# Kernel tuning notes

Measured on AMD Instinct MI355X. Metric: run time of the kernel, lower is better.

## Reference

```python
import jax, jax.numpy as jnp
import numpy as np

B, S, I, H = 32, 512, 512, 1024

def _xavier(key, shape):
    fan_in, fan_out = shape[0], shape[1]
    a = jnp.sqrt(6.0 / (fan_in + fan_out))
    return jax.random.uniform(key, shape, jnp.float32, -a, a)

def setup_inputs() -> dict:
    key = jax.random.key(0)
    ks = jax.random.split(key, 10)
    inp = {
        'x': jax.random.normal(ks[0], (B, S, I), jnp.float32),
        'h0': jnp.zeros((B, H), jnp.float32),
        'c0': jnp.zeros((B, H), jnp.float32),
        'W_ii': _xavier(ks[1], (I, H)), 'W_hi': _xavier(ks[2], (H, H)), 'b_i': jnp.zeros((H,), jnp.float32),
        'W_if': _xavier(ks[3], (I, H)), 'W_hf': _xavier(ks[4], (H, H)), 'b_f': jnp.zeros((H,), jnp.float32),
        'W_ig': _xavier(ks[5], (I, H)), 'W_hg': _xavier(ks[6], (H, H)), 'b_g': jnp.zeros((H,), jnp.float32),
        'W_io': _xavier(ks[7], (I, H)), 'W_ho': _xavier(ks[8], (H, H)), 'b_o': jnp.zeros((H,), jnp.float32),
    }
    return inp

def _lstm(x, h0, c0, W_ii, W_hi, b_i, W_if, W_hf, b_f, W_ig, W_hg, b_g, W_io, W_ho, b_o):
    # Precompute input-to-hidden projections for all timesteps (big fused GEMMs).
    xi = jnp.einsum('bsi,ih->sbh', x, W_ii) + b_i  # (S,B,H)
    xf = jnp.einsum('bsi,ih->sbh', x, W_if) + b_f
    xg = jnp.einsum('bsi,ih->sbh', x, W_ig) + b_g
    xo = jnp.einsum('bsi,ih->sbh', x, W_io) + b_o

    def step(carry, gates_t):
        h, c = carry
        xi_t, xf_t, xg_t, xo_t = gates_t
        i_t = jax.nn.sigmoid(xi_t + h @ W_hi)
        f_t = jax.nn.sigmoid(xf_t + h @ W_hf)
        g_t = jnp.tanh(xg_t + h @ W_hg)
        o_t = jax.nn.sigmoid(xo_t + h @ W_ho)
        c_new = f_t * c + i_t * g_t
        h_new = o_t * jnp.tanh(c_new)
        return (h_new, c_new), (h_new, f_t, i_t, o_t, g_t, c_new)

    (hT, cT), (hs, fs, is_, os, gs, cs) = jax.lax.scan(step, (h0, c0), (xi, xf, xg, xo))
    hidden_seq = jnp.transpose(hs, (1, 0, 2))  # (B,S,H)
    return hidden_seq, hT, cT, fs, is_, os, gs, cs

def reference(x, h0, c0, W_ii, W_hi, b_i, W_if, W_hf, b_f, W_ig, W_hg, b_g, W_io, W_ho, b_o):
    return _lstm(x, h0, c0, W_ii, W_hi, b_i, W_if, W_hf, b_f, W_ig, W_hg, b_g, W_io, W_ho, b_o)
```

## Files before the change

kernel.cpp:

```cpp
#include <hip/hip_runtime.h>
#include <stdint.h>

#define S_LEN 512
#define BATCH 32
#define IDIM 512
#define HDIM 1024
#define NBLK 64

typedef __attribute__((ext_vector_type(8))) short bf16x8;
typedef __attribute__((ext_vector_type(4))) float f32x4;

typedef const __attribute__((address_space(1))) unsigned int as1_uint;
typedef __attribute__((address_space(3))) unsigned int as3_uint;

__device__ __forceinline__ unsigned short f2bf(float f) {
  unsigned int u = __float_as_uint(f);
  u = (u + 0x7fffu + ((u >> 16) & 1u)) >> 16;
  return (unsigned short)u;
}

__device__ __forceinline__ void gld_lds16(const void* g, void* l) {
  __builtin_amdgcn_global_load_lds((as1_uint*)g, (as3_uint*)l, 16, 0, 0);
}

__device__ __forceinline__ float sigm(float x) { return 1.f / (1.f + __expf(-x)); }
__device__ __forceinline__ float tanh_f(float x) { return 1.f - 2.f / (__expf(2.f * x) + 1.f); }

__global__ void k_cast_x(const float* __restrict__ src, unsigned short* __restrict__ dst, int n8) {
  int i0 = blockIdx.x * blockDim.x + threadIdx.x;
  int stride = gridDim.x * blockDim.x;
  for (int i = i0; i < n8; i += stride) {
    const float4* s4 = (const float4*)(src + (size_t)i * 8);
    float4 a = s4[0], b = s4[1];
    bf16x8 v;
    v[0] = (short)f2bf(a.x); v[1] = (short)f2bf(a.y); v[2] = (short)f2bf(a.z); v[3] = (short)f2bf(a.w);
    v[4] = (short)f2bf(b.x); v[5] = (short)f2bf(b.y); v[6] = (short)f2bf(b.z); v[7] = (short)f2bf(b.w);
    *(bf16x8*)(dst + (size_t)i * 8) = v;
  }
}

__global__ void k_tcast_w(const float* __restrict__ src, unsigned short* __restrict__ dst, int K) {
  __shared__ float t[64][65];
  int k0 = blockIdx.x * 64, h0 = blockIdx.y * 64;
  int tid = threadIdx.x;
#pragma unroll 4
  for (int j = 0; j < 16; ++j) {
    int idx = j * 256 + tid;
    int kl = idx >> 6, hl = idx & 63;
    t[kl][hl] = src[(size_t)(k0 + kl) * HDIM + h0 + hl];
  }
  __syncthreads();
  int hl = tid >> 2, kg = tid & 3;
  unsigned short* drow = dst + (size_t)(h0 + hl) * K + k0 + kg * 16;
#pragma unroll
  for (int jj = 0; jj < 4; ++jj) {
    ushort4 v;
    v.x = f2bf(t[kg * 16 + jj * 4 + 0][hl]);
    v.y = f2bf(t[kg * 16 + jj * 4 + 1][hl]);
    v.z = f2bf(t[kg * 16 + jj * 4 + 2][hl]);
    v.w = f2bf(t[kg * 16 + jj * 4 + 3][hl]);
    *(ushort4*)(drow + jj * 4) = v;
  }
}

__global__ __launch_bounds__(256) void k_proj(
    const unsigned short* __restrict__ xb, const unsigned short* __restrict__ wib,
    const float* __restrict__ b_i, const float* __restrict__ b_f,
    const float* __restrict__ b_g, const float* __restrict__ b_o,
    float* __restrict__ Xi, float* __restrict__ Xf, float* __restrict__ Xg,
    float* __restrict__ Xo) {
  __shared__ unsigned short As[128 * 64];
  __shared__ unsigned short Bs[128 * 64];
  int tid = threadIdx.x;
  int l = tid & 63, w = tid >> 6;
  int mt = blockIdx.x >> 5, nt = blockIdx.x & 31;
  int m0 = mt * 128, n0 = nt * 128;
  int g = nt >> 3;
  int wm = (w >> 1) * 64, wn = (w & 1) * 64;

  f32x4 acc[4][4];
  for (int mi = 0; mi < 4; ++mi)
    for (int ni = 0; ni < 4; ++ni)
      for (int r = 0; r < 4; ++r) acc[mi][ni][r] = 0.f;

  for (int kt = 0; kt < 8; ++kt) {
    int k0 = kt * 64;
#pragma unroll
    for (int j = 0; j < 4; ++j) {
      int idx = j * 256 + tid;
      int row = idx >> 3, c = idx & 7;
      int sc = c ^ (row & 7);
      gld_lds16(xb + (size_t)(m0 + row) * IDIM + k0 + sc * 8,
                (char*)As + ((j * 256 + (w << 6)) << 4));
      gld_lds16(wib + (size_t)(n0 + row) * IDIM + k0 + sc * 8,
                (char*)Bs + ((j * 256 + (w << 6)) << 4));
    }
    __syncthreads();
#pragma unroll
    for (int kst = 0; kst < 2; ++kst) {
      bf16x8 af[4], bfr[4];
#pragma unroll
      for (int mi = 0; mi < 4; ++mi) {
        int row = wm + mi * 16 + (l & 15);
        int c = (kst << 2) + (l >> 4);
        af[mi] = *(const bf16x8*)((const char*)As + row * 128 + ((c ^ (row & 7)) << 4));
      }
#pragma unroll
      for (int ni = 0; ni < 4; ++ni) {
        int row = wn + ni * 16 + (l & 15);
        int c = (kst << 2) + (l >> 4);
        bfr[ni] = *(const bf16x8*)((const char*)Bs + row * 128 + ((c ^ (row & 7)) << 4));
      }
#pragma unroll
      for (int mi = 0; mi < 4; ++mi)
#pragma unroll
        for (int ni = 0; ni < 4; ++ni)
          acc[mi][ni] = __builtin_amdgcn_mfma_f32_16x16x32_bf16(af[mi], bfr[ni], acc[mi][ni], 0, 0, 0);
    }
    __syncthreads();
  }

  const float* bias = g == 0 ? b_i : g == 1 ? b_f : g == 2 ? b_g : b_o;
  float* dst = g == 0 ? Xi : g == 1 ? Xf : g == 2 ? Xg : Xo;
#pragma unroll
  for (int ni = 0; ni < 4; ++ni) {
    int n = n0 + wn + ni * 16 + (l & 15);
    int h = n & 1023;
    float bv = bias[h];
#pragma unroll
    for (int mi = 0; mi < 4; ++mi)
#pragma unroll
      for (int r = 0; r < 4; ++r) {
        int m = m0 + wm + mi * 16 + ((l >> 4) << 2) + r;
        int b = m >> 9, s = m & 511;
        dst[(size_t)(s * BATCH + b) * HDIM + h] = acc[mi][ni][r] + bv;
      }
  }
}

__global__ __launch_bounds__(256, 1) void k_rnn(
    const unsigned short* __restrict__ whb, const float* __restrict__ h0,
    const float* __restrict__ c0, char* __restrict__ hbufA,
    char* __restrict__ hbufB, unsigned int* __restrict__ cnt,
    const float* __restrict__ Xi, const float* __restrict__ Xf,
    const float* __restrict__ Xg, const float* __restrict__ Xo,
    float* __restrict__ csw, float* __restrict__ hseq, float* __restrict__ hT,
    float* __restrict__ cT) {
  __shared__ char lds[40960];
  const int ACT = 32768;

  const int tid = threadIdx.x;
  const int w = tid >> 6, l = tid & 63;
  const int ln = l & 15, lk = l >> 4;
  const int bid = blockIdx.x;

  float* isw = (float*)Xi; float* fsw = (float*)Xf;
  float* gsw = (float*)Xg; float* osw = (float*)Xo;
  const float* XW = (w == 0) ? Xi : (w == 1) ? Xf : (w == 2) ? Xg : Xo;

  bf16x8 Breg[4][8];
#pragma unroll
  for (int g = 0; g < 4; ++g)
#pragma unroll
    for (int j = 0; j < 8; ++j)
      Breg[g][j] = *(const bf16x8*)(whb + (((size_t)(g << 10) + (bid << 4) + ln) << 10) +
                                    ((w << 3) + j) * 32 + (lk << 3));

  const int b = tid >> 3, hp = tid & 7;
  const int gh = (bid << 4) + (hp << 1);
  const int fks = gh >> 5, fmt = b >> 4;
  const int flk = ((gh & 31) >> 3);
  const int foff = (((fks << 1) + fmt) << 10) + (flk << 8) + ((b & 15) << 4) + ((hp & 3) << 2);

  float2 c = *(const float2*)&c0[((size_t)b << 10) + gh];

  {
    float2 hv = *(const float2*)&h0[((size_t)b << 10) + gh];
    unsigned int pv = (unsigned int)f2bf(hv.x) | ((unsigned int)f2bf(hv.y) << 16);
    __hip_atomic_store((unsigned int*)(hbufA + foff), pv, __ATOMIC_RELAXED,
                       __HIP_MEMORY_SCOPE_AGENT);
    asm volatile("s_waitcnt vmcnt(0)" ::: "memory");
    __syncthreads();
    if (tid == 0)
      __hip_atomic_fetch_add(cnt + ((bid & 7) << 5), 1u, __ATOMIC_RELAXED,
                             __HIP_MEMORY_SCOPE_AGENT);
  }

  for (int t = 0; t < S_LEN; ++t) {
    const char* hin = (t & 1) ? hbufB : hbufA;
    char* hout = (t & 1) ? hbufA : hbufB;

    float xp[2][4];
    {
      const float* xb_ = XW + (((size_t)(t << 5)) << 10) + (bid << 4) + ln;
#pragma unroll
      for (int mt = 0; mt < 2; ++mt)
#pragma unroll
        for (int r = 0; r < 4; ++r)
          xp[mt][r] = xb_[((size_t)((mt << 4) + (lk << 2) + r)) << 10];
    }

    {
      const unsigned int need = 8u * (unsigned int)(t + 1);
      const unsigned int* cp = cnt + ((l & 7) << 5);
      while (true) {
        unsigned int v = __hip_atomic_load(cp, __ATOMIC_RELAXED, __HIP_MEMORY_SCOPE_AGENT);
        if (__all((l < 8) ? (int)(v >= need) : 1)) break;
        __builtin_amdgcn_s_sleep(1);
      }
    }
    __builtin_amdgcn_sched_barrier(0);

    bf16x8 a[8][2];
#pragma unroll
    for (int j = 0; j < 8; ++j)
#pragma unroll
      for (int mt = 0; mt < 2; ++mt) {
        const char* ap = hin + (((((w << 3) + j) << 1) + mt) << 10) + (l << 4);
        asm volatile("global_load_dwordx4 %0, %1, off sc0 sc1"
                     : "=v"(a[j][mt]) : "v"(ap) : "memory");
      }
    asm volatile("s_waitcnt vmcnt(0)" ::: "memory");
    __builtin_amdgcn_sched_barrier(0);

    f32x4 acc[4][2];
#pragma unroll
    for (int g = 0; g < 4; ++g)
#pragma unroll
      for (int mt = 0; mt < 2; ++mt)
#pragma unroll
        for (int r = 0; r < 4; ++r) acc[g][mt][r] = 0.f;
#pragma unroll
    for (int j = 0; j < 8; ++j)
#pragma unroll
      for (int mt = 0; mt < 2; ++mt)
#pragma unroll
        for (int g = 0; g < 4; ++g)
          acc[g][mt] = __builtin_amdgcn_mfma_f32_16x16x32_bf16(a[j][mt], Breg[g][j],
                                                               acc[g][mt], 0, 0, 0);

#pragma unroll
    for (int g = 0; g < 4; ++g)
#pragma unroll
      for (int mt = 0; mt < 2; ++mt)
        *(f32x4*)(lds + (((((w << 2) + g) << 1) + mt) << 10) + (l << 4)) = acc[g][mt];
    __syncthreads();

#pragma unroll
    for (int mt = 0; mt < 2; ++mt) {
      f32x4 s = *(const f32x4*)(lds + ((((0 * 4 + w) << 1) + mt) << 10) + (l << 4));
#pragma unroll
      for (int kw = 1; kw < 4; ++kw) {
        f32x4 p = *(const f32x4*)(lds + ((((kw * 4 + w) << 1) + mt) << 10) + (l << 4));
#pragma unroll
        for (int r = 0; r < 4; ++r) s[r] += p[r];
      }
#pragma unroll
      for (int r = 0; r < 4; ++r) {
        float pre = s[r] + xp[mt][r];
        float act = (w == 2) ? tanh_f(pre) : sigm(pre);
        *(float*)(lds + ACT + ((((w << 5) + (mt << 4) + (lk << 2) + r) << 4) + ln) * 4) = act;
      }
    }
    __syncthreads();

    float2 iv = *(const float2*)(lds + ACT + ((((0 << 5) + b) << 4) + (hp << 1)) * 4);
    float2 fv = *(const float2*)(lds + ACT + ((((1 << 5) + b) << 4) + (hp << 1)) * 4);
    float2 gv = *(const float2*)(lds + ACT + ((((2 << 5) + b) << 4) + (hp << 1)) * 4);
    float2 ov = *(const float2*)(lds + ACT + ((((3 << 5) + b) << 4) + (hp << 1)) * 4);

    c.x = fv.x * c.x + iv.x * gv.x;
    c.y = fv.y * c.y + iv.y * gv.y;
    float h0v = ov.x * tanh_f(c.x), h1v = ov.y * tanh_f(c.y);

    if (t < S_LEN - 1) {
      unsigned int pv = (unsigned int)f2bf(h0v) | ((unsigned int)f2bf(h1v) << 16);
      __hip_atomic_store((unsigned int*)(hout + foff), pv, __ATOMIC_RELAXED,
                         __HIP_MEMORY_SCOPE_AGENT);
      asm volatile("s_waitcnt vmcnt(0)" ::: "memory");
      __syncthreads();
      if (tid == 0)
        __hip_atomic_fetch_add(cnt + ((bid & 7) << 5), 1u, __ATOMIC_RELAXED,
                               __HIP_MEMORY_SCOPE_AGENT);
    }

    size_t oo = (((size_t)(t << 5) + b) << 10) + gh;
    *(float2*)(isw + oo) = iv;
    *(float2*)(fsw + oo) = fv;
    *(float2*)(gsw + oo) = gv;
    *(float2*)(osw + oo) = ov;
    *(float2*)(csw + oo) = c;
    *(float2*)(hseq + (((size_t)(b << 9) + t) << 10) + gh) = make_float2(h0v, h1v);
    if (t == S_LEN - 1) {
      *(float2*)(hT + (((size_t)b) << 10) + gh) = make_float2(h0v, h1v);
      *(float2*)(cT + (((size_t)b) << 10) + gh) = c;
    }
  }
}

extern "C" void kernel_launch(void* const* d_in, const int* in_sizes, int n_in,
                              void* d_out, int out_size, void* d_ws, size_t ws_size,
                              hipStream_t stream) {
  const float* x = (const float*)d_in[0];
  const float* h0 = (const float*)d_in[1];
  const float* c0 = (const float*)d_in[2];
  const float* Wi[4] = {(const float*)d_in[3], (const float*)d_in[6], (const float*)d_in[9], (const float*)d_in[12]};
  const float* Wh[4] = {(const float*)d_in[4], (const float*)d_in[7], (const float*)d_in[10], (const float*)d_in[13]};
  const float* bias[4] = {(const float*)d_in[5], (const float*)d_in[8], (const float*)d_in[11], (const float*)d_in[14]};

  float* out = (float*)d_out;
  float* R0 = out;
  float* R1 = out + 16777216;
  float* R2 = R1 + 32768;
  float* R3 = R2 + 32768;
  float* R4 = R3 + 16777216;
  float* R5 = R4 + 16777216;
  float* R6 = R5 + 16777216;
  float* R7 = R6 + 16777216;
  float* Xg_[4] = {R4, R3, R6, R5};

  char* ws = (char*)d_ws;
  unsigned short* whb = (unsigned short*)ws;
  unsigned short* wib = (unsigned short*)(ws + 8388608);
  char* hbufA = ws + 12582912;
  char* hbufB = ws + 12648448;
  unsigned int* cnt = (unsigned int*)(ws + 12713984);

  unsigned short* xb = (unsigned short*)R0;

  hipMemsetAsync(cnt, 0, 1024, stream);
  k_cast_x<<<2048, 256, 0, stream>>>(x, xb, (BATCH * S_LEN * IDIM) / 8);
  for (int g = 0; g < 4; ++g) {
    k_tcast_w<<<dim3(8, 16), 256, 0, stream>>>(Wi[g], wib + (size_t)g * 1024 * 512, 512);
    k_tcast_w<<<dim3(16, 16), 256, 0, stream>>>(Wh[g], whb + (size_t)g * 1024 * 1024, 1024);
  }
  k_proj<<<4096, 256, 0, stream>>>(xb, wib, bias[0], bias[1], bias[2], bias[3],
                                   Xg_[0], Xg_[1], Xg_[2], Xg_[3]);
  k_rnn<<<NBLK, 256, 0, stream>>>(whb, h0, c0, hbufA, hbufB, cnt,
                                  Xg_[0], Xg_[1], Xg_[2], Xg_[3],
                                  R7, R0, R1, R2);
}
```

Measured before the change: 2.119 ms.

## Split recurrent LSTM work by batch halves so blocks sync in smaller groups

Each block now handles 16 batch rows and 32 hidden units across all four gates, instead of all 32 batch rows and 16 hidden units. Block parity selects the batch half. Each block waits only on the four counters for its own batch half rather than all eight, and reads half as much h from the exchange buffer per step. The cost is twice as many resident weight registers, which are pinned to AGPRs through an asm constraint. The activation staging area is also padded to a row stride of 34 floats to cut LDS bank conflicts.

New measurement: 1.945 ms. 8.2% less time.

```diff
diff --git a/kernel.cpp b/kernel.cpp
--- a/kernel.cpp
+++ b/kernel.cpp
@@ -146,44 +146,54 @@
     const float* __restrict__ Xg, const float* __restrict__ Xo,
     float* __restrict__ csw, float* __restrict__ hseq, float* __restrict__ hT,
     float* __restrict__ cT) {
-  __shared__ char lds[40960];
+  __shared__ char lds[41472];
   const int ACT = 32768;
 
   const int tid = threadIdx.x;
   const int w = tid >> 6, l = tid & 63;
   const int ln = l & 15, lk = l >> 4;
   const int bid = blockIdx.x;
+  const int dm = bid & 1, hb = bid >> 1;
 
   float* isw = (float*)Xi; float* fsw = (float*)Xf;
   float* gsw = (float*)Xg; float* osw = (float*)Xo;
   const float* XW = (w == 0) ? Xi : (w == 1) ? Xf : (w == 2) ? Xg : Xo;
 
-  bf16x8 Breg[4][8];
+  bf16x8 Breg[8][8];
 #pragma unroll
   for (int g = 0; g < 4; ++g)
 #pragma unroll
+    for (int hh = 0; hh < 2; ++hh)
+#pragma unroll
+      for (int j = 0; j < 8; ++j) {
+        const size_t row = (size_t)((g << 10) + (hb << 5) + (hh << 4) + ln);
+        Breg[g * 2 + hh][j] =
+            *(const bf16x8*)(whb + (row << 10) + (w << 8) + (j << 5) + (lk << 3));
+      }
+#pragma unroll
+  for (int nt = 0; nt < 8; ++nt)
+#pragma unroll
     for (int j = 0; j < 8; ++j)
-      Breg[g][j] = *(const bf16x8*)(whb + (((size_t)(g << 10) + (bid << 4) + ln) << 10) +
-                                    ((w << 3) + j) * 32 + (lk << 3));
-
-  const int b = tid >> 3, hp = tid & 7;
-  const int gh = (bid << 4) + (hp << 1);
-  const int fks = gh >> 5, fmt = b >> 4;
-  const int flk = ((gh & 31) >> 3);
-  const int foff = (((fks << 1) + fmt) << 10) + (flk << 8) + ((b & 15) << 4) + ((hp & 3) << 2);
-
-  float2 c = *(const float2*)&c0[((size_t)b << 10) + gh];
+      asm volatile("" : "+a"(Breg[nt][j]));
+
+  const int pb = tid >> 4, hp = tid & 15;
+  const int bg = (dm << 4) + pb;
+  const int gh = (hb << 5) + (hp << 1);
+  const int o = hp << 1;
+  const int foff = (dm << 15) + (hb << 10) + ((o >> 3) << 8) + (pb << 4) + ((o & 7) << 1);
+  unsigned int* const myflag = cnt + (((dm << 2) + (hb & 3)) << 5);
+
+  float2 c = *(const float2*)&c0[((size_t)bg << 10) + gh];
 
   {
-    float2 hv = *(const float2*)&h0[((size_t)b << 10) + gh];
+    float2 hv = *(const float2*)&h0[((size_t)bg << 10) + gh];
     unsigned int pv = (unsigned int)f2bf(hv.x) | ((unsigned int)f2bf(hv.y) << 16);
     __hip_atomic_store((unsigned int*)(hbufA + foff), pv, __ATOMIC_RELAXED,
                        __HIP_MEMORY_SCOPE_AGENT);
     asm volatile("s_waitcnt vmcnt(0)" ::: "memory");
     __syncthreads();
     if (tid == 0)
-      __hip_atomic_fetch_add(cnt + ((bid & 7) << 5), 1u, __ATOMIC_RELAXED,
-                             __HIP_MEMORY_SCOPE_AGENT);
+      __hip_atomic_fetch_add(myflag, 1u, __ATOMIC_RELAXED, __HIP_MEMORY_SCOPE_AGENT);
   }
 
   for (int t = 0; t < S_LEN; ++t) {
@@ -192,82 +202,76 @@
 
     float xp[2][4];
     {
-      const float* xb_ = XW + (((size_t)(t << 5)) << 10) + (bid << 4) + ln;
-#pragma unroll
-      for (int mt = 0; mt < 2; ++mt)
+      const float* xb_ = XW + ((size_t)((t << 5) + (dm << 4)) << 10) + (hb << 5) + ln;
+#pragma unroll
+      for (int hh = 0; hh < 2; ++hh)
 #pragma unroll
         for (int r = 0; r < 4; ++r)
-          xp[mt][r] = xb_[((size_t)((mt << 4) + (lk << 2) + r)) << 10];
+          xp[hh][r] = xb_[((size_t)((lk << 2) + r) << 10) + (hh << 4)];
     }
 
     {
       const unsigned int need = 8u * (unsigned int)(t + 1);
-      const unsigned int* cp = cnt + ((l & 7) << 5);
+      const unsigned int* cp = cnt + (((dm << 2) + (l & 3)) << 5);
       while (true) {
         unsigned int v = __hip_atomic_load(cp, __ATOMIC_RELAXED, __HIP_MEMORY_SCOPE_AGENT);
-        if (__all((l < 8) ? (int)(v >= need) : 1)) break;
+        if (__all((l < 4) ? (int)(v >= need) : 1)) break;
         __builtin_amdgcn_s_sleep(1);
       }
     }
     __builtin_amdgcn_sched_barrier(0);
 
-    bf16x8 a[8][2];
-#pragma unroll
-    for (int j = 0; j < 8; ++j)
-#pragma unroll
-      for (int mt = 0; mt < 2; ++mt) {
-        const char* ap = hin + (((((w << 3) + j) << 1) + mt) << 10) + (l << 4);
-        asm volatile("global_load_dwordx4 %0, %1, off sc0 sc1"
-                     : "=v"(a[j][mt]) : "v"(ap) : "memory");
-      }
+    bf16x8 a[8];
+    const char* abase = hin + (dm << 15);
+#pragma unroll
+    for (int j = 0; j < 8; ++j) {
+      const char* ap = abase + (((w << 3) + j) << 10) + (l << 4);
+      asm volatile("global_load_dwordx4 %0, %1, off sc0 sc1"
+                   : "=v"(a[j]) : "v"(ap) : "memory");
+    }
     asm volatile("s_waitcnt vmcnt(0)" ::: "memory");
     __builtin_amdgcn_sched_barrier(0);
 
-    f32x4 acc[4][2];
-#pragma unroll
-    for (int g = 0; g < 4; ++g)
-#pragma unroll
-      for (int mt = 0; mt < 2; ++mt)
-#pragma unroll
-        for (int r = 0; r < 4; ++r) acc[g][mt][r] = 0.f;
+    f32x4 acc[8];
+#pragma unroll
+    for (int nt = 0; nt < 8; ++nt)
+#pragma unroll
+      for (int r = 0; r < 4; ++r) acc[nt][r] = 0.f;
 #pragma unroll
     for (int j = 0; j < 8; ++j)
 #pragma unroll
-      for (int mt = 0; mt < 2; ++mt)
-#pragma unroll
-        for (int g = 0; g < 4; ++g)
-          acc[g][mt] = __builtin_amdgcn_mfma_f32_16x16x32_bf16(a[j][mt], Breg[g][j],
-                                                               acc[g][mt], 0, 0, 0);
-
-#pragma unroll
-    for (int g = 0; g < 4; ++g)
-#pragma unroll
-      for (int mt = 0; mt < 2; ++mt)
-        *(f32x4*)(lds + (((((w << 2) + g) << 1) + mt) << 10) + (l << 4)) = acc[g][mt];
-    __syncthreads();
-
-#pragma unroll
-    for (int mt = 0; mt < 2; ++mt) {
-      f32x4 s = *(const f32x4*)(lds + ((((0 * 4 + w) << 1) + mt) << 10) + (l << 4));
+      for (int nt = 0; nt < 8; ++nt)
+        acc[nt] = __builtin_amdgcn_mfma_f32_16x16x32_bf16(a[j], Breg[nt][j], acc[nt], 0, 0, 0);
+
+#pragma unroll
+    for (int nt = 0; nt < 8; ++nt)
+      *(f32x4*)(lds + (((w << 3) + nt) << 10) + (l << 4)) = acc[nt];
+    __syncthreads();
+
+#pragma unroll
+    for (int hh = 0; hh < 2; ++hh) {
+      const int nt = (w << 1) + hh;
+      f32x4 s = *(const f32x4*)(lds + (nt << 10) + (l << 4));
 #pragma unroll
       for (int kw = 1; kw < 4; ++kw) {
-        f32x4 p = *(const f32x4*)(lds + ((((kw * 4 + w) << 1) + mt) << 10) + (l << 4));
+        f32x4 p = *(const f32x4*)(lds + (((kw << 3) + nt) << 10) + (l << 4));
 #pragma unroll
         for (int r = 0; r < 4; ++r) s[r] += p[r];
       }
 #pragma unroll
       for (int r = 0; r < 4; ++r) {
-        float pre = s[r] + xp[mt][r];
+        float pre = s[r] + xp[hh][r];
         float act = (w == 2) ? tanh_f(pre) : sigm(pre);
-        *(float*)(lds + ACT + ((((w << 5) + (mt << 4) + (lk << 2) + r) << 4) + ln) * 4) = act;
-      }
-    }
-    __syncthreads();
-
-    float2 iv = *(const float2*)(lds + ACT + ((((0 << 5) + b) << 4) + (hp << 1)) * 4);
-    float2 fv = *(const float2*)(lds + ACT + ((((1 << 5) + b) << 4) + (hp << 1)) * 4);
-    float2 gv = *(const float2*)(lds + ACT + ((((2 << 5) + b) << 4) + (hp << 1)) * 4);
-    float2 ov = *(const float2*)(lds + ACT + ((((3 << 5) + b) << 4) + (hp << 1)) * 4);
+        ((float*)(lds + ACT))[((w << 4) + (lk << 2) + r) * 34 + (hh << 4) + ln] = act;
+      }
+    }
+    __syncthreads();
+
+    const float* af = (const float*)(lds + ACT);
+    float2 iv = *(const float2*)&af[(0 * 16 + pb) * 34 + o];
+    float2 fv = *(const float2*)&af[(1 * 16 + pb) * 34 + o];
+    float2 gv = *(const float2*)&af[(2 * 16 + pb) * 34 + o];
+    float2 ov = *(const float2*)&af[(3 * 16 + pb) * 34 + o];
 
     c.x = fv.x * c.x + iv.x * gv.x;
     c.y = fv.y * c.y + iv.y * gv.y;
@@ -280,20 +284,19 @@
       asm volatile("s_waitcnt vmcnt(0)" ::: "memory");
       __syncthreads();
       if (tid == 0)
-        __hip_atomic_fetch_add(cnt + ((bid & 7) << 5), 1u, __ATOMIC_RELAXED,
-                               __HIP_MEMORY_SCOPE_AGENT);
-    }
-
-    size_t oo = (((size_t)(t << 5) + b) << 10) + gh;
+        __hip_atomic_fetch_add(myflag, 1u, __ATOMIC_RELAXED, __HIP_MEMORY_SCOPE_AGENT);
+    }
+
+    size_t oo = ((size_t)((t << 5) + bg) << 10) + gh;
     *(float2*)(isw + oo) = iv;
     *(float2*)(fsw + oo) = fv;
     *(float2*)(gsw + oo) = gv;
     *(float2*)(osw + oo) = ov;
     *(float2*)(csw + oo) = c;
-    *(float2*)(hseq + (((size_t)(b << 9) + t) << 10) + gh) = make_float2(h0v, h1v);
+    *(float2*)(hseq + (((size_t)(bg << 9) + t) << 10) + gh) = make_float2(h0v, h1v);
     if (t == S_LEN - 1) {
-      *(float2*)(hT + (((size_t)b) << 10) + gh) = make_float2(h0v, h1v);
-      *(float2*)(cT + (((size_t)b) << 10) + gh) = c;
+      *(float2*)(hT + ((size_t)bg << 10) + gh) = make_float2(h0v, h1v);
+      *(float2*)(cT + ((size_t)bg << 10) + gh) = c;
     }
   }
 }
```
